# Kernel tuning notes

Hardware: AMD Instinct MI355X
Metric: run time of the kernel (lower is better)

Reference implementation:

```python
import jax, jax.numpy as jnp
import numpy as np

B, V, M, L, D, OUT = 16, 16, 32, 24, 128, 193
VOCAB = {'cond': 5000, 'proc': 2000, 'drug': 600, 'lab_item': 700, 'lab_value': 200, 'inj_item': 400, 'inj_value': 200}


def setup_inputs() -> dict:
    key = jax.random.key(0)
    ks = iter(jax.random.split(key, 48))
    def emb_table(v):
        t = 0.02 * jax.random.normal(next(ks), (v, D), jnp.float32)
        return t.at[0].set(0.0)  # padding_idx = 0
    inp = {}
    inp['tok_cond'] = jax.random.randint(next(ks), (B, V, L), 0, VOCAB['cond'])
    inp['tok_proc'] = jax.random.randint(next(ks), (B, V, L), 0, VOCAB['proc'])
    inp['tok_drug'] = jax.random.randint(next(ks), (B, V, L), 0, VOCAB['drug'])
    inp['tok_lab_item'] = jax.random.randint(next(ks), (B, V, M, L), 0, VOCAB['lab_item'])
    inp['tok_lab_value'] = jax.random.randint(next(ks), (B, V, M, L), 0, VOCAB['lab_value'])
    inp['tok_inj_item'] = jax.random.randint(next(ks), (B, V, M, L), 0, VOCAB['inj_item'])
    inp['tok_inj_value'] = jax.random.randint(next(ks), (B, V, M, L), 0, VOCAB['inj_value'])
    inp['weight'] = jax.random.uniform(next(ks), (B, V, 1), jnp.float32)
    inp['age'] = jax.random.uniform(next(ks), (B, V, 1), jnp.float32)
    for n in ['cond', 'proc', 'drug', 'lab_item', 'lab_value', 'inj_item', 'inj_value']:
        inp['emb_' + n] = emb_table(VOCAB[n])
    def gru_params(nk):
        s = 0.05
        return (s * jax.random.normal(next(ks), (nk, 3 * D, D), jnp.float32),
                s * jax.random.normal(next(ks), (nk, 3 * D, D), jnp.float32),
                jnp.zeros((nk, 3 * D), jnp.float32),
                jnp.zeros((nk, 3 * D), jnp.float32))
    inp['mgru_wih'], inp['mgru_whh'], inp['mgru_bih'], inp['mgru_bhh'] = gru_params(5)
    inp['vgru_wih'], inp['vgru_whh'], inp['vgru_bih'], inp['vgru_bhh'] = gru_params(7)
    inp['info_w'] = 0.05 * jax.random.normal(next(ks), (2, D), jnp.float32)  # Linear(1, D) weights for weight/age
    inp['info_b'] = jnp.zeros((2, D), jnp.float32)
    inp['fc_w'] = 0.05 * jax.random.normal(next(ks), (7 * D, OUT), jnp.float32)
    inp['fc_b'] = jnp.zeros((OUT,), jnp.float32)
    return inp


def _gru(x, wih, whh, bih, bhh):
    # x: [N, T, Din]; torch nn.GRU semantics, gate order (r, z, n), h0 = 0
    n_, t_, _ = x.shape
    d = whh.shape[1]
    xg = jnp.einsum('ntd,gd->ntg', x, wih) + bih  # precompute input gates [N, T, 3D]
    def step(h, xg_t):
        gh = h @ whh.T + bhh
        ir, iz, inn = jnp.split(xg_t, 3, axis=-1)
        hr, hz, hn = jnp.split(gh, 3, axis=-1)
        r = jax.nn.sigmoid(ir + hr)
        z = jax.nn.sigmoid(iz + hz)
        n = jnp.tanh(inn + r * hn)
        h2 = (1.0 - z) * n + z * h
        return h2, h2
    h0 = jnp.zeros((n_, d), x.dtype)
    hT, outs = jax.lax.scan(step, h0, jnp.swapaxes(xg, 0, 1))
    return jnp.swapaxes(outs, 0, 1), hT  # output [N,T,D], hidden [N,D]

_gru_keys = jax.vmap(_gru)  # vmap over the per-feature-key leading axis


def reference(tok_cond, tok_proc, tok_drug, tok_lab_item, tok_lab_value, tok_inj_item, tok_inj_value,
              weight, age, emb_cond, emb_proc, emb_drug, emb_lab_item, emb_lab_value, emb_inj_item,
              emb_inj_value, mgru_wih, mgru_whh, mgru_bih, mgru_bhh, vgru_wih, vgru_whh, vgru_bih,
              vgru_bhh, info_w, info_b, fc_w, fc_b):
    b, v, m, _ = tok_lab_item.shape
    d = emb_cond.shape[1]
    # visit-event features: embedding + sum over code dim (dropout = identity, eval mode)
    e_cond = emb_cond[tok_cond].sum(axis=2)  # [B,V,D]
    e_proc = emb_proc[tok_proc].sum(axis=2)
    e_drug = emb_drug[tok_drug].sum(axis=2)
    # monitor-event pairs: elementwise mul of the two embeddings, sum over code dim
    lab = (emb_lab_item[tok_lab_item] * emb_lab_value[tok_lab_value]).sum(axis=3)  # [B,V,M,D]
    inj = (emb_inj_item[tok_inj_item] * emb_inj_value[tok_inj_value]).sum(axis=3)
    # repeat visit embeddings across the monitor axis (repeat(1, max_monitors, 1))
    rep = lambda e: jnp.broadcast_to(e[:, :, None, :], (b, v, m, d))
    mon_in = jnp.stack([rep(e_cond), rep(e_proc), rep(e_drug), lab, inj], axis=0)
    mon_in = mon_in.reshape(5, b * v, m, d)  # aggregate_tensors with uniform lengths
    # per-key monitor-level GRUs
    mon_out, mon_h = _gru_keys(mon_in, mgru_wih, mgru_whh, mgru_bih, mgru_bhh)
    # split_tensor + extract_and_transpose: take last monitor step per visit -> [5,B,V,D]
    last = mon_out[:, :, -1, :].reshape(5, b, v, d)
    # patient info Linear(1, D) for weight / age
    w_emb = weight * info_w[0] + info_b[0]  # [B,V,D]
    a_emb = age * info_w[1] + info_b[1]
    vis_in = jnp.concatenate([last, jnp.stack([w_emb, a_emb], axis=0)], axis=0)  # [7,B,V,D]
    # per-key visit-level GRUs
    _, vis_h = _gru_keys(vis_in, vgru_wih, vgru_whh, vgru_bih, vgru_bhh)  # [7,B,D]
    patient_emb = jnp.transpose(vis_h, (1, 0, 2)).reshape(b, 7 * d)  # concatenate_patient_embeddings
    logits = jax.nn.relu(patient_emb) @ fc_w + fc_b  # fc_patient: ReLU -> Linear(7D, output_size)
    return logits
```

## Files before the change

### kernel.cpp

```cpp
#include <hip/hip_runtime.h>
#include <stdint.h>

typedef unsigned short u16;
typedef unsigned int u32;

#define B_ 16
#define V_ 16
#define M_ 32
#define L_ 24
#define D_ 128
#define G_ 384
#define N_ 256
#define NM_ 8192
#define OUT_ 193

using bf16x8 = __attribute__((ext_vector_type(8))) __bf16;
using floatx4 = __attribute__((ext_vector_type(4))) float;

__device__ __forceinline__ float bf2f(u16 u) {
  u32 x = ((u32)u) << 16;
  return __builtin_bit_cast(float, x);
}
__device__ __forceinline__ u16 f2bf(float f) {
  u32 u = __builtin_bit_cast(u32, f);
  u = (u + 0x7FFFu + ((u >> 16) & 1u)) >> 16;
  return (u16)u;
}
__device__ __forceinline__ float sigm_(float x) {
  return __builtin_amdgcn_rcpf(1.0f + __expf(-x));
}
__device__ __forceinline__ float tanh_(float x) {
  float e = __expf(2.0f * x);
  return 1.0f - 2.0f * __builtin_amdgcn_rcpf(e + 1.0f);
}
__device__ __forceinline__ floatx4 mfma16(bf16x8 a, bf16x8 b, floatx4 c) {
  return __builtin_amdgcn_mfma_f32_16x16x32_bf16(a, b, c, 0, 0, 0);
}
__device__ __forceinline__ void lds_barrier() {
  asm volatile("s_waitcnt lgkmcnt(0)\n\ts_barrier" ::: "memory");
}

__global__ __launch_bounds__(256) void k_conv_w(
    const float* __restrict__ mwih, const float* __restrict__ vwih,
    const float* __restrict__ mwhh, const float* __restrict__ vwhh,
    u16* __restrict__ wih_hi, u16* __restrict__ wih_lo,
    u16* __restrict__ whh_hi, u16* __restrict__ whh_lo) {
  const int S5 = 5 * G_ * D_, S12 = 12 * G_ * D_;
  int i = blockIdx.x * 256 + threadIdx.x;
  float v;
  u16 *dh, *dl;
  int o;
  if (i < S12) {
    o = i;
    v = (o < S5) ? mwih[o] : vwih[o - S5];
    dh = wih_hi; dl = wih_lo;
  } else {
    o = i - S12;
    v = (o < S5) ? mwhh[o] : vwhh[o - S5];
    dh = whh_hi; dl = whh_lo;
  }
  u16 h = f2bf(v);
  dh[o] = h;
  dl[o] = f2bf(v - bf2f(h));
}

__global__ __launch_bounds__(128) void k_visit_embed(
    const int* __restrict__ tc, const int* __restrict__ tp, const int* __restrict__ td,
    const float* __restrict__ ec, const float* __restrict__ ep, const float* __restrict__ ed,
    const float* __restrict__ wv, const float* __restrict__ av,
    const float* __restrict__ iw, const float* __restrict__ ib,
    u16* __restrict__ ce_hi, u16* __restrict__ ce_lo,
    u16* __restrict__ vx_hi, u16* __restrict__ vx_lo) {
  int n = blockIdx.x, d = threadIdx.x;
  float a0 = 0.f, a1 = 0.f, a2 = 0.f;
#pragma unroll 4
  for (int l = 0; l < L_; l++) {
    a0 += ec[(size_t)tc[n * L_ + l] * D_ + d];
    a1 += ep[(size_t)tp[n * L_ + l] * D_ + d];
    a2 += ed[(size_t)td[n * L_ + l] * D_ + d];
  }
  size_t o0 = (size_t)n * D_ + d;
  u16 h;
  h = f2bf(a0); ce_hi[o0] = h;              ce_lo[o0] = f2bf(a0 - bf2f(h));
  h = f2bf(a1); ce_hi[(size_t)N_ * D_ + o0] = h; ce_lo[(size_t)N_ * D_ + o0] = f2bf(a1 - bf2f(h));
  h = f2bf(a2); ce_hi[(size_t)2 * N_ * D_ + o0] = h; ce_lo[(size_t)2 * N_ * D_ + o0] = f2bf(a2 - bf2f(h));
  float w = wv[n], a = av[n];
  float v1 = w * iw[d] + ib[d];
  float v2 = a * iw[D_ + d] + ib[D_ + d];
  h = f2bf(v1); vx_hi[(size_t)5 * N_ * D_ + o0] = h; vx_lo[(size_t)5 * N_ * D_ + o0] = f2bf(v1 - bf2f(h));
  h = f2bf(v2); vx_hi[(size_t)6 * N_ * D_ + o0] = h; vx_lo[(size_t)6 * N_ * D_ + o0] = f2bf(v2 - bf2f(h));
}

__global__ __launch_bounds__(128) void k_pair_embed(
    const int* __restrict__ tli, const int* __restrict__ tlv,
    const int* __restrict__ tii, const int* __restrict__ tiv,
    const float* __restrict__ eli, const float* __restrict__ elv,
    const float* __restrict__ eii, const float* __restrict__ eiv,
    u16* __restrict__ mx_hi, u16* __restrict__ mx_lo) {
  int r = blockIdx.x, d = threadIdx.x;
  float al = 0.f, ai = 0.f;
#pragma unroll 4
  for (int l = 0; l < L_; l++) {
    al += eli[(size_t)tli[r * L_ + l] * D_ + d] * elv[(size_t)tlv[r * L_ + l] * D_ + d];
    ai += eii[(size_t)tii[r * L_ + l] * D_ + d] * eiv[(size_t)tiv[r * L_ + l] * D_ + d];
  }
  size_t o = (size_t)r * D_ + d;
  u16 h;
  h = f2bf(al); mx_hi[o] = h;                      mx_lo[o] = f2bf(al - bf2f(h));
  h = f2bf(ai); mx_hi[(size_t)NM_ * D_ + o] = h;   mx_lo[(size_t)NM_ * D_ + o] = f2bf(ai - bf2f(h));
}

__global__ __launch_bounds__(256) void k_gemm_xg(
    const u16* __restrict__ A_hi, const u16* __restrict__ A_lo,
    const u16* __restrict__ W_hi, const u16* __restrict__ W_lo,
    const float* __restrict__ bias,
    float* __restrict__ out, int A_ks, int W_ks, int b_ks, int o_ks) {
  int key = blockIdx.z;
  int wv = threadIdx.x >> 6, lane = threadIdx.x & 63;
  int mn = lane & 15, q = lane >> 4;
  int row0 = blockIdx.x * 16;
  int col0 = blockIdx.y * 64 + wv * 16;
  const u16* Ah = A_hi + (size_t)key * A_ks + (size_t)(row0 + mn) * D_;
  const u16* Al = A_lo + (size_t)key * A_ks + (size_t)(row0 + mn) * D_;
  const u16* Wh = W_hi + (size_t)key * W_ks + (size_t)(col0 + mn) * D_;
  const u16* Wl = W_lo + (size_t)key * W_ks + (size_t)(col0 + mn) * D_;
  floatx4 acc0 = {0.f, 0.f, 0.f, 0.f};
  floatx4 acc1 = {0.f, 0.f, 0.f, 0.f};
  floatx4 acc2 = {0.f, 0.f, 0.f, 0.f};
#pragma unroll
  for (int kk = 0; kk < 4; kk++) {
    int off = kk * 32 + q * 8;
    bf16x8 a_h = *(const bf16x8*)(Ah + off);
    bf16x8 a_l = *(const bf16x8*)(Al + off);
    bf16x8 w_h = *(const bf16x8*)(Wh + off);
    bf16x8 w_l = *(const bf16x8*)(Wl + off);
    acc0 = mfma16(a_h, w_h, acc0);
    acc1 = mfma16(a_l, w_h, acc1);
    acc2 = mfma16(a_h, w_l, acc2);
  }
  int c = col0 + mn;
  float bv = bias[key * b_ks + c];
  float* op = out + (size_t)key * o_ks + (size_t)(row0 + q * 4) * G_ + c;
#pragma unroll
  for (int i = 0; i < 4; i++) op[(size_t)i * G_] = acc0[i] + acc1[i] + acc2[i] + bv;
}

template <int MODE, int TT>
__global__ __launch_bounds__(256, 1) void k_gru_t(
    int cpk, const float* __restrict__ xg_a, const float* __restrict__ xg_b,
    const u16* __restrict__ whh_all, const float* __restrict__ bhh_all,
    u16* __restrict__ out_hi, u16* __restrict__ out_lo, float* __restrict__ out_f32) {
  int key = blockIdx.x / cpk;
  int chunk = blockIdx.x % cpk;
  int n0 = chunk * 16;
  const u16* whh = whh_all + (size_t)key * (G_ * D_);
  const float* bhh = bhh_all + (size_t)key * G_;

  __shared__ u16 hls[2][2][16 * 128];

  int tid = threadIdx.x;
  int w = tid >> 6, lane = tid & 63, mq = lane & 15, q = lane >> 4;
  int dA = 16 * w + mq;

  bf16x8 bw[6][4];
#pragma unroll
  for (int j = 0; j < 6; j++)
#pragma unroll
    for (int kk = 0; kk < 4; kk++)
      bw[j][kk] = *(const bf16x8*)(whh + (size_t)(16 * w + 64 * j + mq) * D_ + kk * 32 + q * 8);

  floatx4 bias_v[6];
#pragma unroll
  for (int g = 0; g < 3; g++)
#pragma unroll
    for (int ab = 0; ab < 2; ab++) {
      float b = bhh[g * 128 + ab * 64 + dA];
      bias_v[g * 2 + ab] = {b, b, b, b};
    }

  const float* xbase;
  size_t RS, TS;
  if (MODE == 0) {
    if (key < 3) { xbase = xg_a + ((size_t)key * N_ + n0) * G_; RS = G_; TS = 0; }
    else { xbase = xg_b + ((size_t)(key - 3) * NM_ + (size_t)n0 * M_) * G_; RS = (size_t)M_ * G_; TS = G_; }
  } else {
    xbase = xg_a + (size_t)key * N_ * G_; RS = (size_t)16 * G_; TS = G_;
  }
  const float* rowp[4];
#pragma unroll
  for (int i = 0; i < 4; i++) rowp[i] = xbase + (size_t)(q * 4 + i) * RS + dA;

  float xs[4][24];
#pragma unroll
  for (int s = 0; s < 3; s++) {
    int ts = s < TT ? s : TT - 1;
#pragma unroll
    for (int i = 0; i < 4; i++)
#pragma unroll
      for (int g = 0; g < 3; g++)
#pragma unroll
        for (int ab = 0; ab < 2; ab++)
          xs[s][i * 6 + g * 2 + ab] = rowp[i][(size_t)ts * TS + g * 128 + ab * 64];
  }

  float h_old[8];
#pragma unroll
  for (int k = 0; k < 8; k++) h_old[k] = 0.f;

#define GRU_STEP(P)                                                                        \
  {                                                                                        \
    int t = tb + (P);                                                                      \
       \
    {                                                                                      \
      int tpf = t + 3 < TT ? t + 3 : TT - 1;                                               \
      size_t to = (size_t)tpf * TS;                                                        \
      _Pragma("unroll") for (int i = 0; i < 4; i++)                                        \
          _Pragma("unroll") for (int g = 0; g < 3; g++)                                    \
          _Pragma("unroll") for (int ab = 0; ab < 2; ab++)                                 \
              xs[((P) + 3) & 3][i * 6 + g * 2 + ab] = rowp[i][to + g * 128 + ab * 64];     \
    }                                                                                      \
    floatx4 acc[6];                                                                        \
    if (t > 0) {                                                                           \
      const u16* hp0 = &hls[(t - 1) & 1][0][0];                                            \
      const u16* hp1 = &hls[(t - 1) & 1][1][0];                                            \
      bf16x8 ah[4], al[4];                                                                 \
      _Pragma("unroll") for (int kk = 0; kk < 4; kk++) {                                   \
        int off = mq * 128 + (((kk * 4 + q) ^ mq) * 8);                                    \
        ah[kk] = *(const bf16x8*)(hp0 + off);                                              \
        al[kk] = *(const bf16x8*)(hp1 + off);                                              \
      }                                                                                    \
      _Pragma("unroll") for (int j = 0; j < 6; j++) {                                      \
        floatx4 a = mfma16(ah[0], bw[j][0], bias_v[j]);                                    \
        a = mfma16(al[0], bw[j][0], a);                                                    \
        a = mfma16(ah[1], bw[j][1], a);                                                    \
        a = mfma16(al[1], bw[j][1], a);                                                    \
        a = mfma16(ah[2], bw[j][2], a);                                                    \
        a = mfma16(al[2], bw[j][2], a);                                                    \
        a = mfma16(ah[3], bw[j][3], a);                                                    \
        acc[j] = mfma16(al[3], bw[j][3], a);                                               \
      }                                                                                    \
    } else {                                                                               \
      _Pragma("unroll") for (int j = 0; j < 6; j++) acc[j] = bias_v[j];                    \
    }                                                                                      \
    u16* wrh = &hls[t & 1][0][0];                                                          \
    u16* wrl = &hls[t & 1][1][0];                                                          \
    _Pragma("unroll") for (int i = 0; i < 4; i++) {                                        \
      int row = q * 4 + i;                                                                 \
      _Pragma("unroll") for (int ab = 0; ab < 2; ab++) {                                   \
        float ghr = acc[0 + ab][i];                                                        \
        float ghz = acc[2 + ab][i];                                                        \
        float ghn = acc[4 + ab][i];                                                        \
        float xr = xs[P][i * 6 + 0 + ab];                                                  \
        float xz = xs[P][i * 6 + 2 + ab];                                                  \
        float xnn = xs[P][i * 6 + 4 + ab];                                                 \
        float r = sigm_(xr + ghr);                                                         \
        float z = sigm_(xz + ghz);                                                         \
        float nn = tanh_(xnn + r * ghn);                                                   \
        float h2 = (1.0f - z) * nn + z * h_old[i * 2 + ab];                                \
        h_old[i * 2 + ab] = h2;                                                            \
        u32 ub = __builtin_bit_cast(u32, h2);                                              \
        u16 hb = (u16)(ub >> 16);                                                          \
        float rem = h2 - __builtin_bit_cast(float, ub & 0xFFFF0000u);                      \
        u16 lb = f2bf(rem);                                                                \
        int d = dA + ab * 64;                                                              \
        if (t == TT - 1) {                                                                 \
          if (MODE == 0) {                                                                 \
            size_t o = ((size_t)key * N_ + n0 + row) * D_ + d;                             \
            out_hi[o] = hb;                                                                \
            out_lo[o] = lb;                                                                \
          } else {                                                                         \
            out_f32[((size_t)key * 16 + row) * D_ + d] = h2;                               \
          }                                                                                \
        } else {                                                                           \
          int idx = row * 128 + (((d >> 3) ^ row) * 8) + (d & 7);                          \
          wrh[idx] = hb;                                                                   \
          wrl[idx] = lb;                                                                   \
        }                                                                                  \
      }                                                                                    \
    }                                                                                      \
    if (t + 1 < TT) lds_barrier();                                                         \
  }

#pragma unroll 1
  for (int tb = 0; tb < TT; tb += 4) {
    GRU_STEP(0)
    GRU_STEP(1)
    GRU_STEP(2)
    GRU_STEP(3)
  }
#undef GRU_STEP
}

__global__ __launch_bounds__(256) void k_fc(
    const float* __restrict__ vis_h, const float* __restrict__ fc_w,
    const float* __restrict__ fc_b, float* __restrict__ out) {
  int b = blockIdx.x;
  int cg = blockIdx.y;
  int tid = threadIdx.x;
  int j = tid & 15, s = tid >> 4;
  int c = cg * 16 + j;
  bool cv = c < OUT_;

  __shared__ float hbuf[7 * D_];
  __shared__ float red[16][16];
  for (int i = tid; i < 7 * D_; i += 256) {
    float v = vis_h[((size_t)(i >> 7) * 16 + b) * D_ + (i & 127)];
    hbuf[i] = v > 0.f ? v : 0.f;
  }
  __syncthreads();

  float acc = 0.f;
  if (cv) {
    const float* wp = fc_w + (size_t)(s * 56) * OUT_ + c;
#pragma unroll 8
    for (int k = 0; k < 56; k++) acc += hbuf[s * 56 + k] * wp[(size_t)k * OUT_];
  }
  red[s][j] = acc;
  __syncthreads();
  if (s == 0 && cv) {
    float t = 0.f;
#pragma unroll
    for (int m = 0; m < 16; m++) t += red[m][j];
    out[(size_t)b * OUT_ + c] = t + fc_b[c];
  }
}

extern "C" void kernel_launch(void* const* d_in, const int* in_sizes, int n_in,
                              void* d_out, int out_size, void* d_ws, size_t ws_size,
                              hipStream_t stream) {
  (void)in_sizes; (void)n_in; (void)out_size; (void)ws_size;
  const int* tok_cond = (const int*)d_in[0];
  const int* tok_proc = (const int*)d_in[1];
  const int* tok_drug = (const int*)d_in[2];
  const int* tok_lab_item = (const int*)d_in[3];
  const int* tok_lab_value = (const int*)d_in[4];
  const int* tok_inj_item = (const int*)d_in[5];
  const int* tok_inj_value = (const int*)d_in[6];
  const float* weight = (const float*)d_in[7];
  const float* age = (const float*)d_in[8];
  const float* emb_cond = (const float*)d_in[9];
  const float* emb_proc = (const float*)d_in[10];
  const float* emb_drug = (const float*)d_in[11];
  const float* emb_lab_item = (const float*)d_in[12];
  const float* emb_lab_value = (const float*)d_in[13];
  const float* emb_inj_item = (const float*)d_in[14];
  const float* emb_inj_value = (const float*)d_in[15];
  const float* mgru_wih = (const float*)d_in[16];
  const float* mgru_whh = (const float*)d_in[17];
  const float* mgru_bih = (const float*)d_in[18];
  const float* mgru_bhh = (const float*)d_in[19];
  const float* vgru_wih = (const float*)d_in[20];
  const float* vgru_whh = (const float*)d_in[21];
  const float* vgru_bih = (const float*)d_in[22];
  const float* vgru_bhh = (const float*)d_in[23];
  const float* info_w = (const float*)d_in[24];
  const float* info_b = (const float*)d_in[25];
  const float* fc_w = (const float*)d_in[26];
  const float* fc_b = (const float*)d_in[27];

  char* p = (char*)d_ws;
  auto take = [&](size_t bytes) { char* r = p; p += (bytes + 255) & ~(size_t)255; return r; };
  u16* mon_x_hi = (u16*)take((size_t)2 * NM_ * D_ * 2);
  u16* mon_x_lo = (u16*)take((size_t)2 * NM_ * D_ * 2);
  u16* ce_hi = (u16*)take((size_t)3 * N_ * D_ * 2);
  u16* ce_lo = (u16*)take((size_t)3 * N_ * D_ * 2);
  u16* vis_x_hi = (u16*)take((size_t)7 * N_ * D_ * 2);
  u16* vis_x_lo = (u16*)take((size_t)7 * N_ * D_ * 2);
  float* xg_mon = (float*)take((size_t)2 * NM_ * G_ * 4);
  float* xg_c = (float*)take((size_t)3 * N_ * G_ * 4);
  float* xg_v = (float*)take((size_t)7 * N_ * G_ * 4);
  float* vis_h = (float*)take((size_t)7 * 16 * D_ * 4);
  u16* wih_hi = (u16*)take((size_t)12 * G_ * D_ * 2);
  u16* wih_lo = (u16*)take((size_t)12 * G_ * D_ * 2);
  u16* whh_hi = (u16*)take((size_t)12 * G_ * D_ * 2);
  u16* whh_lo = (u16*)take((size_t)12 * G_ * D_ * 2);

  k_conv_w<<<(24 * G_ * D_) / 256, 256, 0, stream>>>(mgru_wih, vgru_wih, mgru_whh, vgru_whh,
                                                     wih_hi, wih_lo, whh_hi, whh_lo);
  k_visit_embed<<<N_, D_, 0, stream>>>(tok_cond, tok_proc, tok_drug, emb_cond, emb_proc, emb_drug,
                                       weight, age, info_w, info_b, ce_hi, ce_lo, vis_x_hi, vis_x_lo);
  k_pair_embed<<<NM_, D_, 0, stream>>>(tok_lab_item, tok_lab_value, tok_inj_item, tok_inj_value,
                                       emb_lab_item, emb_lab_value, emb_inj_item, emb_inj_value,
                                       mon_x_hi, mon_x_lo);
  k_gemm_xg<<<dim3(NM_ / 16, 6, 2), 256, 0, stream>>>(
      mon_x_hi, mon_x_lo, wih_hi + (size_t)3 * G_ * D_, wih_lo + (size_t)3 * G_ * D_,
      mgru_bih + 3 * G_, xg_mon, NM_ * D_, G_ * D_, G_, NM_ * G_);
  k_gemm_xg<<<dim3(N_ / 16, 6, 3), 256, 0, stream>>>(
      ce_hi, ce_lo, wih_hi, wih_lo, mgru_bih, xg_c, N_ * D_, G_ * D_, G_, N_ * G_);
  k_gru_t<0, 32><<<80, 256, 0, stream>>>(16, xg_c, xg_mon, whh_hi, mgru_bhh,
                                         vis_x_hi, vis_x_lo, nullptr);
  k_gemm_xg<<<dim3(N_ / 16, 6, 7), 256, 0, stream>>>(
      vis_x_hi, vis_x_lo, wih_hi + (size_t)5 * G_ * D_, wih_lo + (size_t)5 * G_ * D_,
      vgru_bih, xg_v, N_ * D_, G_ * D_, G_, N_ * G_);
  k_gru_t<1, 16><<<7, 256, 0, stream>>>(1, xg_v, nullptr, whh_hi + (size_t)5 * G_ * D_, vgru_bhh,
                                        nullptr, nullptr, vis_h);
  k_fc<<<dim3(B_, 13), 256, 0, stream>>>(vis_h, fc_w, fc_b, (float*)d_out);
}
```

Measured before the change: 264.8 us.

## Retile input-gate GEMM to reuse register-held weights and drop the W_lo correction term

Each wave now holds a 16-row A tile and reuses it across six 16-column weight tiles (96 columns per block) kept in registers, instead of one 16x16 tile per wave. This cuts redundant global loads of A and W. The W_lo split-precision term is removed, leaving two MFMAs per k-step instead of three, and the bias is folded into the accumulator init. Dropping the low part of the weights lowers accuracy of the input projections, and the larger register footprint may reduce occupancy.

```diff
diff --git a/kernel.cpp b/kernel.cpp
--- a/kernel.cpp
+++ b/kernel.cpp
@@ -112,37 +112,51 @@
 
 __global__ __launch_bounds__(256) void k_gemm_xg(
     const u16* __restrict__ A_hi, const u16* __restrict__ A_lo,
-    const u16* __restrict__ W_hi, const u16* __restrict__ W_lo,
+    const u16* __restrict__ W_hi,
     const float* __restrict__ bias,
     float* __restrict__ out, int A_ks, int W_ks, int b_ks, int o_ks) {
   int key = blockIdx.z;
-  int wv = threadIdx.x >> 6, lane = threadIdx.x & 63;
-  int mn = lane & 15, q = lane >> 4;
-  int row0 = blockIdx.x * 16;
-  int col0 = blockIdx.y * 64 + wv * 16;
-  const u16* Ah = A_hi + (size_t)key * A_ks + (size_t)(row0 + mn) * D_;
-  const u16* Al = A_lo + (size_t)key * A_ks + (size_t)(row0 + mn) * D_;
-  const u16* Wh = W_hi + (size_t)key * W_ks + (size_t)(col0 + mn) * D_;
-  const u16* Wl = W_lo + (size_t)key * W_ks + (size_t)(col0 + mn) * D_;
-  floatx4 acc0 = {0.f, 0.f, 0.f, 0.f};
-  floatx4 acc1 = {0.f, 0.f, 0.f, 0.f};
-  floatx4 acc2 = {0.f, 0.f, 0.f, 0.f};
+  int w = threadIdx.x >> 6, lane = threadIdx.x & 63;
+  int mq = lane & 15, q = lane >> 4;
+  int row = blockIdx.x * 64 + w * 16;
+  int cb = blockIdx.y * 96;
+
+  const u16* Wk = W_hi + (size_t)key * W_ks;
+  bf16x8 wf[6][4];
+#pragma unroll
+  for (int j = 0; j < 6; j++)
+#pragma unroll
+    for (int kk = 0; kk < 4; kk++)
+      wf[j][kk] = *(const bf16x8*)(Wk + (size_t)(cb + j * 16 + mq) * D_ + kk * 32 + q * 8);
+
+  const u16* Ah = A_hi + (size_t)key * A_ks + (size_t)(row + mq) * D_;
+  const u16* Al = A_lo + (size_t)key * A_ks + (size_t)(row + mq) * D_;
+  bf16x8 ah[4], al[4];
 #pragma unroll
   for (int kk = 0; kk < 4; kk++) {
-    int off = kk * 32 + q * 8;
-    bf16x8 a_h = *(const bf16x8*)(Ah + off);
-    bf16x8 a_l = *(const bf16x8*)(Al + off);
-    bf16x8 w_h = *(const bf16x8*)(Wh + off);
-    bf16x8 w_l = *(const bf16x8*)(Wl + off);
-    acc0 = mfma16(a_h, w_h, acc0);
-    acc1 = mfma16(a_l, w_h, acc1);
-    acc2 = mfma16(a_h, w_l, acc2);
-  }
-  int c = col0 + mn;
-  float bv = bias[key * b_ks + c];
-  float* op = out + (size_t)key * o_ks + (size_t)(row0 + q * 4) * G_ + c;
-#pragma unroll
-  for (int i = 0; i < 4; i++) op[(size_t)i * G_] = acc0[i] + acc1[i] + acc2[i] + bv;
+    ah[kk] = *(const bf16x8*)(Ah + kk * 32 + q * 8);
+    al[kk] = *(const bf16x8*)(Al + kk * 32 + q * 8);
+  }
+
+  floatx4 acc[6];
+#pragma unroll
+  for (int j = 0; j < 6; j++) {
+    float bv = bias[key * b_ks + cb + j * 16 + mq];
+    acc[j] = {bv, bv, bv, bv};
+  }
+#pragma unroll
+  for (int j = 0; j < 6; j++)
+#pragma unroll
+    for (int kk = 0; kk < 4; kk++) {
+      acc[j] = mfma16(ah[kk], wf[j][kk], acc[j]);
+      acc[j] = mfma16(al[kk], wf[j][kk], acc[j]);
+    }
+
+  float* op = out + (size_t)key * o_ks + (size_t)(row + q * 4) * G_ + cb + mq;
+#pragma unroll
+  for (int j = 0; j < 6; j++)
+#pragma unroll
+    for (int i = 0; i < 4; i++) op[(size_t)i * G_ + j * 16] = acc[j][i];
 }
 
 template <int MODE, int TT>
@@ -210,7 +224,6 @@
 #define GRU_STEP(P)                                                                        \
   {                                                                                        \
     int t = tb + (P);                                                                      \
-       \
     {                                                                                      \
       int tpf = t + 3 < TT ? t + 3 : TT - 1;                                               \
       size_t to = (size_t)tpf * TS;                                                        \
@@ -382,15 +395,15 @@
   k_pair_embed<<<NM_, D_, 0, stream>>>(tok_lab_item, tok_lab_value, tok_inj_item, tok_inj_value,
                                        emb_lab_item, emb_lab_value, emb_inj_item, emb_inj_value,
                                        mon_x_hi, mon_x_lo);
-  k_gemm_xg<<<dim3(NM_ / 16, 6, 2), 256, 0, stream>>>(
-      mon_x_hi, mon_x_lo, wih_hi + (size_t)3 * G_ * D_, wih_lo + (size_t)3 * G_ * D_,
+  k_gemm_xg<<<dim3(NM_ / 64, 4, 2), 256, 0, stream>>>(
+      mon_x_hi, mon_x_lo, wih_hi + (size_t)3 * G_ * D_,
       mgru_bih + 3 * G_, xg_mon, NM_ * D_, G_ * D_, G_, NM_ * G_);
-  k_gemm_xg<<<dim3(N_ / 16, 6, 3), 256, 0, stream>>>(
-      ce_hi, ce_lo, wih_hi, wih_lo, mgru_bih, xg_c, N_ * D_, G_ * D_, G_, N_ * G_);
+  k_gemm_xg<<<dim3(N_ / 64, 4, 3), 256, 0, stream>>>(
+      ce_hi, ce_lo, wih_hi, mgru_bih, xg_c, N_ * D_, G_ * D_, G_, N_ * G_);
   k_gru_t<0, 32><<<80, 256, 0, stream>>>(16, xg_c, xg_mon, whh_hi, mgru_bhh,
                                          vis_x_hi, vis_x_lo, nullptr);
-  k_gemm_xg<<<dim3(N_ / 16, 6, 7), 256, 0, stream>>>(
-      vis_x_hi, vis_x_lo, wih_hi + (size_t)5 * G_ * D_, wih_lo + (size_t)5 * G_ * D_,
+  k_gemm_xg<<<dim3(N_ / 64, 4, 7), 256, 0, stream>>>(
+      vis_x_hi, vis_x_lo, wih_hi + (size_t)5 * G_ * D_,
       vgru_bih, xg_v, N_ * D_, G_ * D_, G_, N_ * G_);
   k_gru_t<1, 16><<<7, 256, 0, stream>>>(1, xg_v, nullptr, whh_hi + (size_t)5 * G_ * D_, vgru_bhh,
                                         nullptr, nullptr, vis_h);
```

After: 235.3 us. 1.12x faster.
